# Kernel tuning notes

Hardware: AMD Instinct MI355X
Metric: run time of the kernel (lower is better)

Reference implementation:

```python
import jax, jax.numpy as jnp
import numpy as np

NUM_ENT = 50000
NUM_REL = 64
NUM_TRI = 400000
DIN = 128
DOUT = 128
DREL = 128
NUM_HEAD = 8
DH = DOUT // NUM_HEAD


def setup_inputs() -> dict:
    key = jax.random.key(0)
    ks = jax.random.split(key, 9)
    emb_ent = jax.random.normal(ks[0], (NUM_ENT, DIN), jnp.float32)
    emb_rel = jax.random.normal(ks[1], (NUM_REL, DREL), jnp.float32)
    heads = jax.random.randint(ks[2], (NUM_TRI,), 0, NUM_ENT)
    rels = jax.random.randint(ks[3], (NUM_TRI,), 0, NUM_REL)
    tails = jax.random.randint(ks[4], (NUM_TRI,), 0, NUM_ENT)
    triplets = jnp.stack([heads, rels, tails], axis=-1)
    # xavier-normal-like init (stored as [in, out]; torch Linear applies x @ W.T)
    Wa = jax.random.normal(ks[5], (2 * DIN + DREL, DOUT), jnp.float32) * (2.0 / (2 * DIN + DREL + DOUT)) ** 0.5
    ba = jnp.zeros((DOUT,), jnp.float32)
    attn_vec = jax.random.normal(ks[6], (1, NUM_HEAD, DH), jnp.float32) * 0.1
    Wg = jax.random.normal(ks[7], (DIN + DREL, DOUT), jnp.float32) * (2.0 / (DIN + DREL + DOUT)) ** 0.5
    bg = jnp.zeros((DOUT,), jnp.float32)
    return {"emb_ent": emb_ent, "emb_rel": emb_rel, "triplets": triplets,
            "Wa": Wa, "ba": ba, "attn_vec": attn_vec, "Wg": Wg, "bg": bg}


def reference(emb_ent, emb_rel, triplets, Wa, ba, attn_vec, Wg, bg):
    num_ent = emb_ent.shape[0]
    n_head, d_hid = attn_vec.shape[1], attn_vec.shape[2]
    head, rel, tail = triplets[:, 0], triplets[:, 1], triplets[:, 2]

    # in-degree of each entity (as attention-softmax denominator for self_rel)
    ent_freq = jax.ops.segment_sum(jnp.ones(tail.shape, jnp.float32), tail,
                                   num_segments=num_ent)[:, None]
    # torch adds 1e-16 to all entries iff any entry is zero
    ent_freq = ent_freq + jnp.where(jnp.any(ent_freq == 0.0), 1e-16, 0.0)

    # mean relation embedding of incoming edges per entity -> self-loop relation
    self_rel = jax.ops.segment_sum(emb_rel[rel], tail, num_segments=num_ent) / ent_freq

    # append self-loops: one per entity
    emb_rels = jnp.concatenate([emb_rel[rel], self_rel], axis=0)       # [E+N, dr]
    ar = jnp.arange(num_ent)
    head_all = jnp.concatenate([head, ar], axis=0)                     # [E+N]
    tail_all = jnp.concatenate([tail, ar], axis=0)                     # [E+N]

    # attention logits per edge per head
    feat_att = jnp.concatenate([emb_ent[tail_all], emb_ent[head_all], emb_rels], axis=-1)
    h = jnp.tanh(feat_att @ Wa + ba).reshape(-1, n_head, d_hid)
    attn_raw = jnp.sum(h * attn_vec, axis=-1, keepdims=True)           # [E+N, H, 1]

    # segment softmax over edges sharing a tail (every segment has a self-loop)
    amax = jax.ops.segment_max(attn_raw, tail_all, num_segments=num_ent)
    attn_val = jnp.exp(attn_raw - amax[tail_all])
    asum = jax.ops.segment_sum(attn_val, tail_all, num_segments=num_ent)
    beta = attn_val / (asum[tail_all] + 1e-16)                         # [E+N, H, 1]

    # message projection and weighted aggregation
    msg = (jnp.concatenate([emb_ent[head_all], emb_rels], axis=-1) @ Wg + bg)
    msg = msg.reshape(-1, n_head, d_hid)
    out = jax.ops.segment_sum(beta * msg, tail_all, num_segments=num_ent)
    return out.reshape(num_ent, -1)
```

## Files before the change

### kernel.cpp

```cpp
#include <hip/hip_runtime.h>
#include <math.h>

#define NUM_ENT  50000
#define NUM_REL  64
#define NUM_TRI  400000
#define DIN      128
#define CAP      64

#define PACK_BLOCKS  24
#define SMALL_BLOCKS 64
#define ZERO_BLOCKS  196
#define PREP_BLOCKS  (PACK_BLOCKS + SMALL_BLOCKS + ZERO_BLOCKS)

#define ENT_BLOCKS   782
#define SCAT_BLOCKS  1563
#define MID_BLOCKS   (ENT_BLOCKS + SCAT_BLOCKS)

typedef __attribute__((ext_vector_type(8))) short bf16x8;
typedef __attribute__((ext_vector_type(4))) float f32x4;

__device__ __forceinline__ float4 f4add(float4 a, float4 b) {
    return make_float4(a.x + b.x, a.y + b.y, a.z + b.z, a.w + b.w);
}

__device__ __forceinline__ unsigned short f2bf(float f) {
    unsigned u = __float_as_uint(f);
    unsigned r = ((u >> 16) & 1u) + 0x7fffu;
    return (unsigned short)((u + r) >> 16);
}
__device__ __forceinline__ float bf2f(unsigned short h) {
    return __uint_as_float(((unsigned)h) << 16);
}
__device__ __forceinline__ float4 ldbf4(const unsigned short* p) {
    ushort4 u = *(const ushort4*)p;
    return make_float4(bf2f(u.x), bf2f(u.y), bf2f(u.z), bf2f(u.w));
}
__device__ __forceinline__ void ldbf8(const unsigned short* p, float4* lo, float4* hi) {
    ushort4 u0 = *(const ushort4*)p;
    ushort4 u1 = *(const ushort4*)(p + 4);
    *lo = make_float4(bf2f(u0.x), bf2f(u0.y), bf2f(u0.z), bf2f(u0.w));
    *hi = make_float4(bf2f(u1.x), bf2f(u1.y), bf2f(u1.z), bf2f(u1.w));
}

__device__ __forceinline__ float tanhf_fast(float x) {
    float e = __expf(2.f * x);
    return 1.f - 2.f * __builtin_amdgcn_rcpf(e + 1.f);
}
__device__ __forceinline__ float tanh_dot4(float4 x, float4 av) {
    return tanhf_fast(x.x) * av.x + tanhf_fast(x.y) * av.y +
           tanhf_fast(x.z) * av.z + tanhf_fast(x.w) * av.w;
}

__global__ __launch_bounds__(256) void k_prep(const float* __restrict__ emb_rel,
                                              const float* __restrict__ Wa,
                                              const float* __restrict__ Wg,
                                              unsigned short* __restrict__ Bpack,
                                              unsigned short* __restrict__ TaTg,
                                              int* __restrict__ deg) {
    __shared__ float s[DIN];
    int b = blockIdx.x;
    int tid = threadIdx.x;

    if (b < PACK_BLOCKS) {
        for (int i = 0; i < 8; i++) {
            int idx = b * 2048 + i * 256 + tid;
            int j    = idx & 7;
            int lane = (idx >> 3) & 63;
            int ks   = (idx >> 9) & 3;
            int t    = (idx >> 11) & 7;
            int w    = idx >> 14;
            int k = ks * 32 + ((lane >> 4) << 3) + j;
            int n = t * 16 + (lane & 15);
            const float* W = (w == 0) ? Wa : (w == 1) ? (Wa + 128 * DIN) : Wg;
            Bpack[idx] = f2bf(W[k * DIN + n]);
        }
    } else if (b < PACK_BLOCKS + SMALL_BLOCKS) {
        int row = b - PACK_BLOCKS;
        if (tid < DIN) s[tid] = emb_rel[row * DIN + tid];
        __syncthreads();
        int j = tid & 127;
        const float* W = (tid < 128) ? (Wa + 256 * DIN) : (Wg + 128 * DIN);
        float acc = 0.f;
#pragma unroll 8
        for (int k = 0; k < DIN; k++) acc += s[k] * W[k * DIN + j];
        int pos = row * 256 + 8 * (j >> 2) + (j & 3) + ((tid < 128) ? 0 : 4);
        TaTg[pos] = f2bf(acc);
    } else {
        int idx = (b - PACK_BLOCKS - SMALL_BLOCKS) * 256 + tid;
        if (idx < NUM_ENT) deg[idx] = 0;
    }
}

__global__ __launch_bounds__(256) void k_mid(const float* __restrict__ X,
                                             const unsigned short* __restrict__ Bpack,
                                             const int* __restrict__ trip,
                                             const float* __restrict__ ba,
                                             const float* __restrict__ bg,
                                             unsigned short* __restrict__ Pt,
                                             unsigned short* __restrict__ PhGh,
                                             int* __restrict__ deg,
                                             int2* __restrict__ elist2) {
    __shared__ unsigned short As[64][136];
    int b = blockIdx.x;
    int tid = threadIdx.x;

    if (b < ENT_BLOCKS) {
        int m0 = b * 64;
        for (int i = 0; i < 8; i++) {
            int v = tid + i * 256;
            int row = v >> 5;
            int c4 = v & 31;
            int gr = m0 + row;
            if (gr >= NUM_ENT) gr = NUM_ENT - 1;
            float4 x = *(const float4*)&X[gr * DIN + c4 * 4];
            ushort4 h;
            h.x = f2bf(x.x); h.y = f2bf(x.y); h.z = f2bf(x.z); h.w = f2bf(x.w);
            *(ushort4*)&As[row][c4 * 4] = h;
        }
        __syncthreads();

        int w = tid >> 6;
        int q = tid & 63;
        int quad = q >> 4;
        int lrow = w * 16 + (q & 15);
        int gr = m0 + lrow;

        bf16x8 a[4];
#pragma unroll
        for (int ks = 0; ks < 4; ks++)
            a[ks] = *(const bf16x8*)&As[lrow][ks * 32 + quad * 8];

        const bf16x8* Bp = (const bf16x8*)Bpack;
#pragma unroll
        for (int s = 0; s < 3; s++) {
            f32x4 acc[8];
#pragma unroll
            for (int t = 0; t < 8; t++) acc[t] = (f32x4){0.f, 0.f, 0.f, 0.f};
#pragma unroll
            for (int ks = 0; ks < 4; ks++) {
#pragma unroll
                for (int t = 0; t < 8; t++) {
                    bf16x8 wf = Bp[((s * 8 + t) * 4 + ks) * 64 + q];
                    acc[t] = __builtin_amdgcn_mfma_f32_16x16x32_bf16(wf, a[ks], acc[t], 0, 0, 0);
                }
            }
            if (gr < NUM_ENT) {
#pragma unroll
                for (int t = 0; t < 8; t++) {
                    int n0 = t * 16 + quad * 4;
                    float4 bb = make_float4(0.f, 0.f, 0.f, 0.f);
                    if (s == 0) bb = *(const float4*)&ba[n0];
                    if (s == 2) bb = *(const float4*)&bg[n0];
                    ushort4 o;
                    o.x = f2bf(acc[t][0] + bb.x);
                    o.y = f2bf(acc[t][1] + bb.y);
                    o.z = f2bf(acc[t][2] + bb.z);
                    o.w = f2bf(acc[t][3] + bb.w);
                    if (s == 0) {
                        *(ushort4*)&Pt[gr * DIN + n0] = o;
                    } else {
                        *(ushort4*)&PhGh[gr * 256 + 2 * n0 + ((s == 1) ? 0 : 4)] = o;
                    }
                }
            }
        }
    } else {
        int i = (b - ENT_BLOCKS) * 256 + tid;
        if (i < NUM_TRI) {
            int h = trip[i * 3 + 0];
            int r = trip[i * 3 + 1];
            int t = trip[i * 3 + 2];
            int pos = atomicAdd(&deg[t], 1);
            if (pos < CAP) elist2[t * CAP + pos] = make_int2(h, r);
        }
    }
}

__global__ __launch_bounds__(256) void k_fused(const int2* __restrict__ elist2,
                                               const int* __restrict__ deg_arr,
                                               const unsigned short* __restrict__ Pt,
                                               const unsigned short* __restrict__ PhGh,
                                               const unsigned short* __restrict__ TaTg,
                                               const float* __restrict__ attn_vec,
                                               float* __restrict__ out) {
    int tid = threadIdx.x;
    int g = tid >> 5;
    int q = tid & 31;
    int t = blockIdx.x * 8 + g;
    int deg = deg_arr[t];
    if (deg > CAP) deg = CAP;
    int c = q * 4;

    float4 pt4 = ldbf4(&Pt[t * DIN + c]);
    float4 av4 = *(const float4*)&attn_vec[c];

    float l = 0.f;
    float4 acc = make_float4(0.f, 0.f, 0.f, 0.f);
    float4 sTa = make_float4(0.f, 0.f, 0.f, 0.f);
    float4 sTg = make_float4(0.f, 0.f, 0.f, 0.f);

    const int2* eb = &elist2[t * CAP];
    for (int it = 0; it < deg; it++) {
        int2 hr = eb[it];
        float4 ta, tg, ph, gh;
        ldbf8(&TaTg[hr.y * 256 + q * 8], &ta, &tg);
        ldbf8(&PhGh[hr.x * 256 + q * 8], &ph, &gh);
        sTa = f4add(sTa, ta);
        sTg = f4add(sTg, tg);
        float4 pa = f4add(ph, ta);
        float4 gm = f4add(gh, tg);
        float p = tanh_dot4(f4add(pt4, pa), av4);
        p += __shfl_xor(p, 1);
        p += __shfl_xor(p, 2);
        float w = __expf(p);
        l += w;
        acc.x += w * gm.x; acc.y += w * gm.y; acc.z += w * gm.z; acc.w += w * gm.w;
    }
    {
        float inv = (deg > 0) ? __builtin_amdgcn_rcpf((float)deg) : 0.f;
        float4 pa, gm;
        ldbf8(&PhGh[t * 256 + q * 8], &pa, &gm);
        pa.x += sTa.x * inv; pa.y += sTa.y * inv; pa.z += sTa.z * inv; pa.w += sTa.w * inv;
        gm.x += sTg.x * inv; gm.y += sTg.y * inv; gm.z += sTg.z * inv; gm.w += sTg.w * inv;
        float p = tanh_dot4(f4add(pt4, pa), av4);
        p += __shfl_xor(p, 1);
        p += __shfl_xor(p, 2);
        float w = __expf(p);
        l += w;
        acc.x += w * gm.x; acc.y += w * gm.y; acc.z += w * gm.z; acc.w += w * gm.w;
    }
    float invl = 1.f / (l + 1e-16f);
    *(float4*)&out[t * DIN + c] =
        make_float4(acc.x * invl, acc.y * invl, acc.z * invl, acc.w * invl);
}

extern "C" void kernel_launch(void* const* d_in, const int* in_sizes, int n_in,
                              void* d_out, int out_size, void* d_ws, size_t ws_size,
                              hipStream_t stream) {
    const float* emb_ent  = (const float*)d_in[0];
    const float* emb_rel  = (const float*)d_in[1];
    const int*   trip     = (const int*)d_in[2];
    const float* Wa       = (const float*)d_in[3];
    const float* ba       = (const float*)d_in[4];
    const float* attn_vec = (const float*)d_in[5];
    const float* Wg       = (const float*)d_in[6];
    const float* bg       = (const float*)d_in[7];
    float* out = (float*)d_out;

    unsigned short* wsh = (unsigned short*)d_ws;
    unsigned short* Pt    = wsh;
    unsigned short* PhGh  = wsh + 6400000;
    unsigned short* TaTg  = wsh + 19200000;
    unsigned short* Bpack = wsh + 19216384;
    int*  deg    = (int*)(wsh + 19265536);
    int2* elist2 = (int2*)(deg + 50000);

    k_prep<<<PREP_BLOCKS, 256, 0, stream>>>(emb_rel, Wa, Wg, Bpack, TaTg, deg);

    k_mid<<<MID_BLOCKS, 256, 0, stream>>>(emb_ent, Bpack, trip, ba, bg,
                                          Pt, PhGh, deg, elist2);

    k_fused<<<NUM_ENT / 8, 256, 0, stream>>>(elist2, deg,
                                             Pt, PhGh, TaTg, attn_vec, out);
}
```

Before: 191.2 us.

## Pack edge list into single int, vectorize scatter, split edges across wave halves

The edge list now stores head and relation packed into one 32-bit int (head<<6 | rel) instead of an int2, which halves edge-list traffic. The scatter phase handles four triplets per thread using int4 loads. The fused aggregation kernel now gives each tail one 64-lane wave: it loads the whole edge list with one coalesced read, broadcasts entries by shuffle, and lets the two 32-lane halves process alternating edges before combining partial sums with xor-32 shuffles. This adds more latency hiding per tail and fewer scalar index loads, at the cost of idle lanes for low-degree tails and extra shuffle reductions.

```diff
diff --git a/kernel.cpp b/kernel.cpp
--- a/kernel.cpp
+++ b/kernel.cpp
@@ -13,7 +13,7 @@
 #define PREP_BLOCKS  (PACK_BLOCKS + SMALL_BLOCKS + ZERO_BLOCKS)
 
 #define ENT_BLOCKS   782
-#define SCAT_BLOCKS  1563
+#define SCAT_BLOCKS  391
 #define MID_BLOCKS   (ENT_BLOCKS + SCAT_BLOCKS)
 
 typedef __attribute__((ext_vector_type(8))) short bf16x8;
@@ -99,7 +99,7 @@
                                              unsigned short* __restrict__ Pt,
                                              unsigned short* __restrict__ PhGh,
                                              int* __restrict__ deg,
-                                             int2* __restrict__ elist2) {
+                                             int* __restrict__ elist) {
     __shared__ unsigned short As[64][136];
     int b = blockIdx.x;
     int tid = threadIdx.x;
@@ -165,18 +165,23 @@
             }
         }
     } else {
-        int i = (b - ENT_BLOCKS) * 256 + tid;
-        if (i < NUM_TRI) {
-            int h = trip[i * 3 + 0];
-            int r = trip[i * 3 + 1];
-            int t = trip[i * 3 + 2];
-            int pos = atomicAdd(&deg[t], 1);
-            if (pos < CAP) elist2[t * CAP + pos] = make_int2(h, r);
-        }
-    }
-}
-
-__global__ __launch_bounds__(256) void k_fused(const int2* __restrict__ elist2,
+        int i0 = (b - ENT_BLOCKS) * 1024 + tid * 4;
+        if (i0 < NUM_TRI) {
+            const int4* tp = (const int4*)&trip[i0 * 3];
+            int4 A = tp[0], B4 = tp[1], C4 = tp[2];
+            int hs[4] = {A.x, A.w, B4.z, C4.y};
+            int rs[4] = {A.y, B4.x, B4.w, C4.z};
+            int ts[4] = {A.z, B4.y, C4.x, C4.w};
+#pragma unroll
+            for (int u = 0; u < 4; u++) {
+                int pos = atomicAdd(&deg[ts[u]], 1);
+                if (pos < CAP) elist[ts[u] * CAP + pos] = (hs[u] << 6) | rs[u];
+            }
+        }
+    }
+}
+
+__global__ __launch_bounds__(256) void k_fused(const int* __restrict__ elist,
                                                const int* __restrict__ deg_arr,
                                                const unsigned short* __restrict__ Pt,
                                                const unsigned short* __restrict__ PhGh,
@@ -184,27 +189,32 @@
                                                const float* __restrict__ attn_vec,
                                                float* __restrict__ out) {
     int tid = threadIdx.x;
-    int g = tid >> 5;
-    int q = tid & 31;
-    int t = blockIdx.x * 8 + g;
+    int wv = tid >> 6;
+    int lane = tid & 63;
+    int half = lane >> 5;
+    int q = lane & 31;
+    int t = blockIdx.x * 4 + wv;
     int deg = deg_arr[t];
     if (deg > CAP) deg = CAP;
     int c = q * 4;
 
     float4 pt4 = ldbf4(&Pt[t * DIN + c]);
     float4 av4 = *(const float4*)&attn_vec[c];
+
+    int eall = elist[t * CAP + lane];
 
     float l = 0.f;
     float4 acc = make_float4(0.f, 0.f, 0.f, 0.f);
     float4 sTa = make_float4(0.f, 0.f, 0.f, 0.f);
     float4 sTg = make_float4(0.f, 0.f, 0.f, 0.f);
 
-    const int2* eb = &elist2[t * CAP];
-    for (int it = 0; it < deg; it++) {
-        int2 hr = eb[it];
+    for (int it = half; it < deg; it += 2) {
+        int e = __shfl(eall, it);
+        int h = e >> 6;
+        int r = e & 63;
         float4 ta, tg, ph, gh;
-        ldbf8(&TaTg[hr.y * 256 + q * 8], &ta, &tg);
-        ldbf8(&PhGh[hr.x * 256 + q * 8], &ph, &gh);
+        ldbf8(&TaTg[r * 256 + q * 8], &ta, &tg);
+        ldbf8(&PhGh[h * 256 + q * 8], &ph, &gh);
         sTa = f4add(sTa, ta);
         sTg = f4add(sTg, tg);
         float4 pa = f4add(ph, ta);
@@ -216,6 +226,21 @@
         l += w;
         acc.x += w * gm.x; acc.y += w * gm.y; acc.z += w * gm.z; acc.w += w * gm.w;
     }
+
+    l     += __shfl_xor(l, 32);
+    acc.x += __shfl_xor(acc.x, 32);
+    acc.y += __shfl_xor(acc.y, 32);
+    acc.z += __shfl_xor(acc.z, 32);
+    acc.w += __shfl_xor(acc.w, 32);
+    sTa.x += __shfl_xor(sTa.x, 32);
+    sTa.y += __shfl_xor(sTa.y, 32);
+    sTa.z += __shfl_xor(sTa.z, 32);
+    sTa.w += __shfl_xor(sTa.w, 32);
+    sTg.x += __shfl_xor(sTg.x, 32);
+    sTg.y += __shfl_xor(sTg.y, 32);
+    sTg.z += __shfl_xor(sTg.z, 32);
+    sTg.w += __shfl_xor(sTg.w, 32);
+
     {
         float inv = (deg > 0) ? __builtin_amdgcn_rcpf((float)deg) : 0.f;
         float4 pa, gm;
@@ -230,8 +255,10 @@
         acc.x += w * gm.x; acc.y += w * gm.y; acc.z += w * gm.z; acc.w += w * gm.w;
     }
     float invl = 1.f / (l + 1e-16f);
-    *(float4*)&out[t * DIN + c] =
-        make_float4(acc.x * invl, acc.y * invl, acc.z * invl, acc.w * invl);
+    if (half == 0) {
+        *(float4*)&out[t * DIN + c] =
+            make_float4(acc.x * invl, acc.y * invl, acc.z * invl, acc.w * invl);
+    }
 }
 
 extern "C" void kernel_launch(void* const* d_in, const int* in_sizes, int n_in,
@@ -252,14 +279,14 @@
     unsigned short* PhGh  = wsh + 6400000;
     unsigned short* TaTg  = wsh + 19200000;
     unsigned short* Bpack = wsh + 19216384;
-    int*  deg    = (int*)(wsh + 19265536);
-    int2* elist2 = (int2*)(deg + 50000);
+    int* deg   = (int*)(wsh + 19265536);
+    int* elist = deg + 50000;
 
     k_prep<<<PREP_BLOCKS, 256, 0, stream>>>(emb_rel, Wa, Wg, Bpack, TaTg, deg);
 
     k_mid<<<MID_BLOCKS, 256, 0, stream>>>(emb_ent, Bpack, trip, ba, bg,
-                                          Pt, PhGh, deg, elist2);
-
-    k_fused<<<NUM_ENT / 8, 256, 0, stream>>>(elist2, deg,
+                                          Pt, PhGh, deg, elist);
+
+    k_fused<<<NUM_ENT / 4, 256, 0, stream>>>(elist, deg,
                                              Pt, PhGh, TaTg, attn_vec, out);
 }
```

Result: no change. 189.8 us (-0.7%).
